# Kernel tuning notes

Measured on AMD Instinct MI355X. Metric: run time of the kernel, lower is better.

Reference implementation:

```python
import jax, jax.numpy as jnp
import numpy as np

DT = 0.025    # ms, integration time step
CM = 1.0      # uF/cm^2 membrane capacitance
E_NA, E_K, E_L = 50.0, -77.0, -54.387  # mV reversal potentials

T, N = 8192, 2048


def setup_inputs() -> dict:
    key = jax.random.key(0)
    ks = jax.random.split(key, 5)
    return {
        "input_estim": 5.0 * jax.random.normal(ks[0], (T, N), dtype=jnp.float32),  # uA/cm^2 stim per segment per step
        "V0": -65.0 + 2.0 * jax.random.normal(ks[1], (N,), dtype=jnp.float32),
        "m0": 0.05 + 0.02 * jax.random.uniform(ks[2], (N,), dtype=jnp.float32),
        "h0": 0.60 + 0.05 * jax.random.uniform(ks[3], (N,), dtype=jnp.float32),
        "n0": 0.32 + 0.05 * jax.random.uniform(ks[4], (N,), dtype=jnp.float32),
        "g_na": 120.0 * jnp.ones((N,), jnp.float32),
        "g_k": 36.0 * jnp.ones((N,), jnp.float32),
        "g_l": 0.3 * jnp.ones((N,), jnp.float32),
        "g_ax": 5.0 * jnp.ones((N,), jnp.float32),  # axial coupling conductance between neighbor segments
    }


def _rates(V):
    am = 0.1 * (V + 40.0) / (1.0 - jnp.exp(-(V + 40.0) / 10.0))
    bm = 4.0 * jnp.exp(-(V + 65.0) / 18.0)
    ah = 0.07 * jnp.exp(-(V + 65.0) / 20.0)
    bh = 1.0 / (1.0 + jnp.exp(-(V + 35.0) / 10.0))
    an = 0.01 * (V + 55.0) / (1.0 - jnp.exp(-(V + 55.0) / 10.0))
    bn = 0.125 * jnp.exp(-(V + 65.0) / 80.0)
    return am, bm, ah, bh, an, bn


def reference(input_estim, V0, m0, h0, n0, g_na, g_k, g_l, g_ax):
    def step(state, i_stim):
        V, m, h, n = state
        am, bm, ah, bh, an, bn = _rates(V)
        i_ion = (g_na * m**3 * h * (V - E_NA)
                 + g_k * n**4 * (V - E_K)
                 + g_l * (V - E_L))
        # sealed-end cable: zero-flux boundaries via edge padding
        Vp = jnp.pad(V, (1, 1), mode="edge")
        i_ax = g_ax * (Vp[:-2] + Vp[2:] - 2.0 * V)
        dV = (i_ax + i_stim - i_ion) / CM
        # total transmembrane current (capacitive + ionic) = axial + stim
        mem_cur = CM * dV + i_ion
        new_state = (V + DT * dV,
                     m + DT * (am * (1.0 - m) - bm * m),
                     h + DT * (ah * (1.0 - h) - bh * h),
                     n + DT * (an * (1.0 - n) - bn * n))
        return new_state, (mem_cur, V)

    state0 = (V0, m0, h0, n0)
    (Vf, mf, hf, nf), (mem_currents, mem_voltages) = jax.lax.scan(step, state0, input_estim)
    # (mem_currents_over_time, mem_voltage_over_time, final state)
    return mem_currents, mem_voltages, Vf, mf, hf, nf
```

## Files before the change

kernel.cpp:

```cpp
#include <hip/hip_runtime.h>

typedef unsigned long long u64;
typedef unsigned int u32;

#define TSTEPS 8192
#define NSEG   2048
#define DTC    0.025f

#define KST    28
#define KTAIL  16
#define WAVE   64
#define COWN   8
#define NBLK   (NSEG / COWN)
#define NPH    ((TSTEPS + KST - 1) / KST)
#define JLO    KST
#define LDP    66

constexpr double L2E = 1.4426950408889634074;

#define AM_A ((float)(-0.1 * L2E))
#define CEM  0.018315638888734179f
#define CEH  0.030197383422318501f
#define CEN  0.0040867714384640666f
#define BM_A ((float)(-L2E / 18.0))
#define BM_B ((float)(2.0 - 65.0 * L2E / 18.0))
#define QA   ((float)(-L2E / 80.0))
#define QB   ((float)(-65.0 * L2E / 80.0))
#define CAH  0.2645751311064591f

#define AL(p) __hip_atomic_load((p), __ATOMIC_RELAXED, __HIP_MEMORY_SCOPE_AGENT)
#define AS(p, v) __hip_atomic_store((p), (v), __ATOMIC_RELAXED, __HIP_MEMORY_SCOPE_AGENT)

__device__ __forceinline__ u64 pack_tag(float v, int tag) {
    return ((u64)(u32)tag << 32) | (u64)__float_as_uint(v);
}
__device__ __forceinline__ float lo_f(u64 w) { return __uint_as_float((u32)w); }
__device__ __forceinline__ float bperm(int addr, float v) {
    return __int_as_float(__builtin_amdgcn_ds_bpermute(addr, __float_as_int(v)));
}

template <int KS>
__device__ __forceinline__ void run_phase(
    int p, int b, int j, int s, int sc,
    bool owned, int addrL, int addrR,
    float gna, float gk, float gl, float gax,
    const float* __restrict__ stim, u64* __restrict__ tstate,
    float* __restrict__ out_cur, float* __restrict__ out_volt,
    float* lds, float& V, float& m, float& h, float& n, bool pub)
{
    const int t0 = p * KST;
    const float* sp = stim + (size_t)t0 * NSEG + sc;

    float st[KS];
#pragma unroll
    for (int k = 0; k < KS; ++k)
        st[k] = sp[(size_t)k * NSEG];
    __builtin_amdgcn_sched_barrier(0);

    const bool needLoad = (!owned) || (p == 0);
    const u64* sb = tstate + (size_t)(p & 1) * 4 * NSEG + sc;
    {
        u64 w0 = 0, w1 = 0, w2 = 0, w3 = 0;
        int ok;
        do {
            ok = 1;
            if (needLoad) {
                w0 = AL(sb);            w1 = AL(sb + NSEG);
                w2 = AL(sb + 2 * NSEG); w3 = AL(sb + 3 * NSEG);
                ok = (int)(w0 >> 32) >= p && (int)(w1 >> 32) >= p &&
                     (int)(w2 >> 32) >= p && (int)(w3 >> 32) >= p;
            }
        } while (!__all(ok));
        if (needLoad) {
            V = lo_f(w0); m = lo_f(w1); h = lo_f(w2); n = lo_f(w3);
        }
    }

    float Vl = bperm(addrL, V);
    float Vr = bperm(addrR, V);

    float2* ld2 = (float2*)lds;
#pragma unroll
    for (int k = 0; k < KS; ++k) {
        const float is = st[k];
        const float ax = (Vl + Vr) - 2.0f * V;
        const float mc = __builtin_fmaf(gax, ax, is);
        const float m3 = m * m * m;
        const float n2 = n * n;
        const float i_ion = gna * m3 * h * (V - 50.0f)
                          + gk * (n2 * n2) * (V + 77.0f)
                          + gl * (V + 54.387f);
        const float dV = mc - i_ion;
        const float Vn = __builtin_fmaf(DTC, dV, V);
        const float VlN = bperm(addrL, Vn);
        const float VrN = bperm(addrR, Vn);

        ld2[k * LDP + j] = make_float2(mc, V);

        const float em0 = __builtin_amdgcn_exp2f(V * AM_A);
        const float am  = __builtin_fmaf(0.1f, V, 4.0f) *
                          __builtin_amdgcn_rcpf(__builtin_fmaf(-CEM, em0, 1.0f));
        const float an  = __builtin_fmaf(0.01f, V, 0.55f) *
                          __builtin_amdgcn_rcpf(__builtin_fmaf(-CEN, em0, 1.0f));
        const float bh  = __builtin_amdgcn_rcpf(__builtin_fmaf(CEH, em0, 1.0f));
        const float bm  = __builtin_amdgcn_exp2f(__builtin_fmaf(V, BM_A, BM_B));
        const float q   = __builtin_amdgcn_exp2f(__builtin_fmaf(V, QA, QB));
        const float tq  = CAH * (q * q);
        const float ah  = tq * tq;
        const float bn  = 0.125f * q;

        m = __builtin_fmaf(DTC, __builtin_fmaf(-(am + bm), m, am), m);
        h = __builtin_fmaf(DTC, __builtin_fmaf(-(ah + bh), h, ah), h);
        n = __builtin_fmaf(DTC, __builtin_fmaf(-(an + bn), n, an), n);
        V = Vn; Vl = VlN; Vr = VrN;
    }

    if (pub && owned) {
        u64* pb = tstate + (size_t)((p + 1) & 1) * 4 * NSEG + s;
        AS(pb,            pack_tag(V, p + 1));
        AS(pb + NSEG,     pack_tag(m, p + 1));
        AS(pb + 2 * NSEG, pack_tag(h, p + 1));
        AS(pb + 3 * NSEG, pack_tag(n, p + 1));
    }
    __builtin_amdgcn_sched_barrier(0);

    const int sbase = b * COWN;
#pragma unroll
    for (int base = 0; base < KS * COWN; base += WAVE) {
        const int idx = base + j;
        if (idx < KS * COWN) {
            const int t  = idx >> 3;
            const int sl = idx & 7;
            const float* lp = lds + (size_t)(t * LDP + JLO + sl) * 2;
            const size_t go = (size_t)(t0 + t) * NSEG + (sbase + sl);
            __builtin_nontemporal_store(lp[0], out_cur + go);
            __builtin_nontemporal_store(lp[1], out_volt + go);
        }
    }
}

__global__ __launch_bounds__(WAVE, 1) void hh_persist(
    const float* __restrict__ stim,
    const float* __restrict__ gna_p, const float* __restrict__ gk_p,
    const float* __restrict__ gl_p,  const float* __restrict__ gax_p,
    u64* __restrict__ tstate,
    float* __restrict__ out_cur, float* __restrict__ out_volt,
    float* __restrict__ tail)
{
    const int j = threadIdx.x;
    const int b = blockIdx.x;
    const int s = b * COWN - KST + j;
    const int sc = s < 0 ? 0 : (s > NSEG - 1 ? NSEG - 1 : s);
    const bool owned = (j >= JLO) && (j < JLO + COWN);

    const int jl = (s <= 0)        ? j : (j > 0  ? j - 1 : 0);
    const int jr = (s >= NSEG - 1) ? j : (j < 63 ? j + 1 : 63);
    const int addrL = jl * 4;
    const int addrR = jr * 4;

    const float gna = gna_p[sc], gk = gk_p[sc], gl = gl_p[sc], gax = gax_p[sc];

    __shared__ float lds[KST * LDP * 2];

    float V = 0.f, m = 0.f, h = 0.f, n = 0.f;

    for (int p = 0; p < NPH - 1; ++p)
        run_phase<KST>(p, b, j, s, sc, owned, addrL, addrR, gna, gk, gl, gax,
                       stim, tstate, out_cur, out_volt, lds, V, m, h, n, true);
    run_phase<KTAIL>(NPH - 1, b, j, s, sc, owned, addrL, addrR, gna, gk, gl, gax,
                     stim, tstate, out_cur, out_volt, lds, V, m, h, n, false);

    if (owned) {
        tail[s] = V; tail[NSEG + s] = m;
        tail[2 * NSEG + s] = h; tail[3 * NSEG + s] = n;
    }
}

__global__ void hh_init(const float* __restrict__ V0, const float* __restrict__ m0,
                        const float* __restrict__ h0, const float* __restrict__ n0,
                        u64* __restrict__ tstate)
{
    const int i = blockIdx.x * blockDim.x + threadIdx.x;
    if (i < NSEG) {
        tstate[i]            = pack_tag(V0[i], 0);
        tstate[NSEG + i]     = pack_tag(m0[i], 0);
        tstate[2 * NSEG + i] = pack_tag(h0[i], 0);
        tstate[3 * NSEG + i] = pack_tag(n0[i], 0);
        u64* b1 = tstate + 4 * NSEG;
        const u64 inv = (u64)(u32)0x80000000u << 32;
        b1[i] = inv; b1[NSEG + i] = inv; b1[2 * NSEG + i] = inv; b1[3 * NSEG + i] = inv;
    }
}

extern "C" void kernel_launch(void* const* d_in, const int* in_sizes, int n_in,
                              void* d_out, int out_size, void* d_ws, size_t ws_size,
                              hipStream_t stream)
{
    const float* stim = (const float*)d_in[0];
    const float* V0   = (const float*)d_in[1];
    const float* m0   = (const float*)d_in[2];
    const float* h0   = (const float*)d_in[3];
    const float* n0   = (const float*)d_in[4];
    const float* gna  = (const float*)d_in[5];
    const float* gk   = (const float*)d_in[6];
    const float* gl   = (const float*)d_in[7];
    const float* gax  = (const float*)d_in[8];

    float* out      = (float*)d_out;
    float* out_cur  = out;
    float* out_volt = out + (size_t)TSTEPS * NSEG;
    float* tail     = out + 2 * (size_t)TSTEPS * NSEG;

    u64* tstate = (u64*)d_ws;

    hipLaunchKernelGGL(hh_init, dim3(8), dim3(256), 0, stream,
                       V0, m0, h0, n0, tstate);
    hipLaunchKernelGGL(hh_persist, dim3(NBLK), dim3(WAVE), 0, stream,
                       stim, gna, gk, gl, gax, tstate,
                       out_cur, out_volt, tail);
}
```

Measured before the change: 1.178 ms.

## Prefetch next phase's stimulus before output flush and compact LDS staging buffer

The stimulus loads for the next phase are now issued at the end of the current phase, after publishing state and before the output stores, so their latency overlaps the global stores and the inter-block spin wait instead of stalling the start of each phase. The LDS staging buffer is shrunk to only the owned lanes' values, written conditionally. Register pressure rises because the prefetched stimulus array persists across phases, and the extra phase-specialised instantiation grows code size.

```diff
diff --git a/kernel.cpp b/kernel.cpp
--- a/kernel.cpp
+++ b/kernel.cpp
@@ -14,7 +14,6 @@
 #define NBLK   (NSEG / COWN)
 #define NPH    ((TSTEPS + KST - 1) / KST)
 #define JLO    KST
-#define LDP    66
 
 constexpr double L2E = 1.4426950408889634074;
 
@@ -39,23 +38,17 @@
     return __int_as_float(__builtin_amdgcn_ds_bpermute(addr, __float_as_int(v)));
 }
 
-template <int KS>
+template <int KS, int KN>
 __device__ __forceinline__ void run_phase(
     int p, int b, int j, int s, int sc,
     bool owned, int addrL, int addrR,
     float gna, float gk, float gl, float gax,
     const float* __restrict__ stim, u64* __restrict__ tstate,
     float* __restrict__ out_cur, float* __restrict__ out_volt,
-    float* lds, float& V, float& m, float& h, float& n, bool pub)
+    float2* lbuf, float (&st)[KST],
+    float& V, float& m, float& h, float& n, bool pub)
 {
     const int t0 = p * KST;
-    const float* sp = stim + (size_t)t0 * NSEG + sc;
-
-    float st[KS];
-#pragma unroll
-    for (int k = 0; k < KS; ++k)
-        st[k] = sp[(size_t)k * NSEG];
-    __builtin_amdgcn_sched_barrier(0);
 
     const bool needLoad = (!owned) || (p == 0);
     const u64* sb = tstate + (size_t)(p & 1) * 4 * NSEG + sc;
@@ -79,7 +72,7 @@
     float Vl = bperm(addrL, V);
     float Vr = bperm(addrR, V);
 
-    float2* ld2 = (float2*)lds;
+    const int jo = j - JLO;
 #pragma unroll
     for (int k = 0; k < KS; ++k) {
         const float is = st[k];
@@ -95,7 +88,7 @@
         const float VlN = bperm(addrL, Vn);
         const float VrN = bperm(addrR, Vn);
 
-        ld2[k * LDP + j] = make_float2(mc, V);
+        if (owned) lbuf[k * COWN + jo] = make_float2(mc, V);
 
         const float em0 = __builtin_amdgcn_exp2f(V * AM_A);
         const float am  = __builtin_fmaf(0.1f, V, 4.0f) *
@@ -124,17 +117,23 @@
     }
     __builtin_amdgcn_sched_barrier(0);
 
+    if (KN > 0) {
+        const float* spn = stim + (size_t)(t0 + KST) * NSEG + sc;
+#pragma unroll
+        for (int u = 0; u < KN; ++u)
+            st[u] = spn[(size_t)u * NSEG];
+    }
+    __builtin_amdgcn_sched_barrier(0);
+
     const int sbase = b * COWN;
 #pragma unroll
     for (int base = 0; base < KS * COWN; base += WAVE) {
         const int idx = base + j;
         if (idx < KS * COWN) {
-            const int t  = idx >> 3;
-            const int sl = idx & 7;
-            const float* lp = lds + (size_t)(t * LDP + JLO + sl) * 2;
-            const size_t go = (size_t)(t0 + t) * NSEG + (sbase + sl);
-            __builtin_nontemporal_store(lp[0], out_cur + go);
-            __builtin_nontemporal_store(lp[1], out_volt + go);
+            const float2 v = lbuf[idx];
+            const size_t go = (size_t)(t0 + (idx >> 3)) * NSEG + sbase + (idx & 7);
+            __builtin_nontemporal_store(v.x, out_cur + go);
+            __builtin_nontemporal_store(v.y, out_volt + go);
         }
     }
 }
@@ -160,15 +159,26 @@
 
     const float gna = gna_p[sc], gk = gk_p[sc], gl = gl_p[sc], gax = gax_p[sc];
 
-    __shared__ float lds[KST * LDP * 2];
+    __shared__ float2 lbuf[KST * COWN];
 
     float V = 0.f, m = 0.f, h = 0.f, n = 0.f;
-
-    for (int p = 0; p < NPH - 1; ++p)
-        run_phase<KST>(p, b, j, s, sc, owned, addrL, addrR, gna, gk, gl, gax,
-                       stim, tstate, out_cur, out_volt, lds, V, m, h, n, true);
-    run_phase<KTAIL>(NPH - 1, b, j, s, sc, owned, addrL, addrR, gna, gk, gl, gax,
-                     stim, tstate, out_cur, out_volt, lds, V, m, h, n, false);
+    float st[KST];
+
+#pragma unroll
+    for (int u = 0; u < KST; ++u)
+        st[u] = stim[(size_t)u * NSEG + sc];
+    __builtin_amdgcn_sched_barrier(0);
+
+    for (int p = 0; p < NPH - 2; ++p)
+        run_phase<KST, KST>(p, b, j, s, sc, owned, addrL, addrR,
+                            gna, gk, gl, gax, stim, tstate,
+                            out_cur, out_volt, lbuf, st, V, m, h, n, true);
+    run_phase<KST, KTAIL>(NPH - 2, b, j, s, sc, owned, addrL, addrR,
+                          gna, gk, gl, gax, stim, tstate,
+                          out_cur, out_volt, lbuf, st, V, m, h, n, true);
+    run_phase<KTAIL, 0>(NPH - 1, b, j, s, sc, owned, addrL, addrR,
+                        gna, gk, gl, gax, stim, tstate,
+                        out_cur, out_volt, lbuf, st, V, m, h, n, false);
 
     if (owned) {
         tail[s] = V; tail[NSEG + s] = m;
```

Result: no change. 1.194 ms (+1.4%).

## Widen blocks to four waves with LDS neighbor exchange and staged stimulus

Applied to the files above, without the earlier changes.

Replaces 256 single-wave blocks (8 owned segments, 28-step halos) with 16 blocks of 256 threads that each own 128 segments, using 64-step phases and 64-cell halos on each side. Neighbor voltages are exchanged through shared memory with a __syncthreads every time step instead of wave-local ds_bpermute. Stimulus is staged into LDS with vectorized float4 loads, and outputs are buffered in LDS, then written back coalesced. This reduces redundant halo compute and the number of cross-block sync phases, but adds a block-wide barrier per step and uses only 16 of the device's CUs.

```diff
diff --git a/kernel.cpp b/kernel.cpp
--- a/kernel.cpp
+++ b/kernel.cpp
@@ -7,14 +7,11 @@
 #define NSEG   2048
 #define DTC    0.025f
 
-#define KST    28
-#define KTAIL  16
-#define WAVE   64
-#define COWN   8
+#define NT     256
+#define KST    64
+#define COWN   128
 #define NBLK   (NSEG / COWN)
-#define NPH    ((TSTEPS + KST - 1) / KST)
-#define JLO    KST
-#define LDP    66
+#define NPH    (TSTEPS / KST)
 
 constexpr double L2E = 1.4426950408889634074;
 
@@ -35,111 +32,11 @@
     return ((u64)(u32)tag << 32) | (u64)__float_as_uint(v);
 }
 __device__ __forceinline__ float lo_f(u64 w) { return __uint_as_float((u32)w); }
-__device__ __forceinline__ float bperm(int addr, float v) {
-    return __int_as_float(__builtin_amdgcn_ds_bpermute(addr, __float_as_int(v)));
-}
-
-template <int KS>
-__device__ __forceinline__ void run_phase(
-    int p, int b, int j, int s, int sc,
-    bool owned, int addrL, int addrR,
-    float gna, float gk, float gl, float gax,
-    const float* __restrict__ stim, u64* __restrict__ tstate,
-    float* __restrict__ out_cur, float* __restrict__ out_volt,
-    float* lds, float& V, float& m, float& h, float& n, bool pub)
-{
-    const int t0 = p * KST;
-    const float* sp = stim + (size_t)t0 * NSEG + sc;
-
-    float st[KS];
-#pragma unroll
-    for (int k = 0; k < KS; ++k)
-        st[k] = sp[(size_t)k * NSEG];
-    __builtin_amdgcn_sched_barrier(0);
-
-    const bool needLoad = (!owned) || (p == 0);
-    const u64* sb = tstate + (size_t)(p & 1) * 4 * NSEG + sc;
-    {
-        u64 w0 = 0, w1 = 0, w2 = 0, w3 = 0;
-        int ok;
-        do {
-            ok = 1;
-            if (needLoad) {
-                w0 = AL(sb);            w1 = AL(sb + NSEG);
-                w2 = AL(sb + 2 * NSEG); w3 = AL(sb + 3 * NSEG);
-                ok = (int)(w0 >> 32) >= p && (int)(w1 >> 32) >= p &&
-                     (int)(w2 >> 32) >= p && (int)(w3 >> 32) >= p;
-            }
-        } while (!__all(ok));
-        if (needLoad) {
-            V = lo_f(w0); m = lo_f(w1); h = lo_f(w2); n = lo_f(w3);
-        }
-    }
-
-    float Vl = bperm(addrL, V);
-    float Vr = bperm(addrR, V);
-
-    float2* ld2 = (float2*)lds;
-#pragma unroll
-    for (int k = 0; k < KS; ++k) {
-        const float is = st[k];
-        const float ax = (Vl + Vr) - 2.0f * V;
-        const float mc = __builtin_fmaf(gax, ax, is);
-        const float m3 = m * m * m;
-        const float n2 = n * n;
-        const float i_ion = gna * m3 * h * (V - 50.0f)
-                          + gk * (n2 * n2) * (V + 77.0f)
-                          + gl * (V + 54.387f);
-        const float dV = mc - i_ion;
-        const float Vn = __builtin_fmaf(DTC, dV, V);
-        const float VlN = bperm(addrL, Vn);
-        const float VrN = bperm(addrR, Vn);
-
-        ld2[k * LDP + j] = make_float2(mc, V);
-
-        const float em0 = __builtin_amdgcn_exp2f(V * AM_A);
-        const float am  = __builtin_fmaf(0.1f, V, 4.0f) *
-                          __builtin_amdgcn_rcpf(__builtin_fmaf(-CEM, em0, 1.0f));
-        const float an  = __builtin_fmaf(0.01f, V, 0.55f) *
-                          __builtin_amdgcn_rcpf(__builtin_fmaf(-CEN, em0, 1.0f));
-        const float bh  = __builtin_amdgcn_rcpf(__builtin_fmaf(CEH, em0, 1.0f));
-        const float bm  = __builtin_amdgcn_exp2f(__builtin_fmaf(V, BM_A, BM_B));
-        const float q   = __builtin_amdgcn_exp2f(__builtin_fmaf(V, QA, QB));
-        const float tq  = CAH * (q * q);
-        const float ah  = tq * tq;
-        const float bn  = 0.125f * q;
-
-        m = __builtin_fmaf(DTC, __builtin_fmaf(-(am + bm), m, am), m);
-        h = __builtin_fmaf(DTC, __builtin_fmaf(-(ah + bh), h, ah), h);
-        n = __builtin_fmaf(DTC, __builtin_fmaf(-(an + bn), n, an), n);
-        V = Vn; Vl = VlN; Vr = VrN;
-    }
-
-    if (pub && owned) {
-        u64* pb = tstate + (size_t)((p + 1) & 1) * 4 * NSEG + s;
-        AS(pb,            pack_tag(V, p + 1));
-        AS(pb + NSEG,     pack_tag(m, p + 1));
-        AS(pb + 2 * NSEG, pack_tag(h, p + 1));
-        AS(pb + 3 * NSEG, pack_tag(n, p + 1));
-    }
-    __builtin_amdgcn_sched_barrier(0);
-
-    const int sbase = b * COWN;
-#pragma unroll
-    for (int base = 0; base < KS * COWN; base += WAVE) {
-        const int idx = base + j;
-        if (idx < KS * COWN) {
-            const int t  = idx >> 3;
-            const int sl = idx & 7;
-            const float* lp = lds + (size_t)(t * LDP + JLO + sl) * 2;
-            const size_t go = (size_t)(t0 + t) * NSEG + (sbase + sl);
-            __builtin_nontemporal_store(lp[0], out_cur + go);
-            __builtin_nontemporal_store(lp[1], out_volt + go);
-        }
-    }
-}
-
-__global__ __launch_bounds__(WAVE, 1) void hh_persist(
+__device__ __forceinline__ int clampi(int x) {
+    return x < 0 ? 0 : (x > NSEG - 1 ? NSEG - 1 : x);
+}
+
+__global__ __launch_bounds__(NT, 1) void hh_persist(
     const float* __restrict__ stim,
     const float* __restrict__ gna_p, const float* __restrict__ gk_p,
     const float* __restrict__ gl_p,  const float* __restrict__ gax_p,
@@ -147,30 +44,131 @@
     float* __restrict__ out_cur, float* __restrict__ out_volt,
     float* __restrict__ tail)
 {
-    const int j = threadIdx.x;
-    const int b = blockIdx.x;
-    const int s = b * COWN - KST + j;
-    const int sc = s < 0 ? 0 : (s > NSEG - 1 ? NSEG - 1 : s);
-    const bool owned = (j >= JLO) && (j < JLO + COWN);
-
-    const int jl = (s <= 0)        ? j : (j > 0  ? j - 1 : 0);
-    const int jr = (s >= NSEG - 1) ? j : (j < 63 ? j + 1 : 63);
-    const int addrL = jl * 4;
-    const int addrR = jr * 4;
+    const int tid = threadIdx.x;
+    const int b   = blockIdx.x;
+    const int s   = b * COWN - KST + tid;
+    const int sc  = clampi(s);
+    const int wid = tid >> 6;
+    const bool ownedWave = (wid == 1) || (wid == 2);
+    const int jl = (s <= 0)        ? tid : (tid > 0      ? tid - 1 : tid);
+    const int jr = (s >= NSEG - 1) ? tid : (tid < NT - 1 ? tid + 1 : tid);
 
     const float gna = gna_p[sc], gk = gk_p[sc], gl = gl_p[sc], gax = gax_p[sc];
 
-    __shared__ float lds[KST * LDP * 2];
+    __shared__ float  stimS[KST * NT];
+    __shared__ float2 outS[KST * COWN];
+    __shared__ float  vx[2][NT];
 
     float V = 0.f, m = 0.f, h = 0.f, n = 0.f;
 
-    for (int p = 0; p < NPH - 1; ++p)
-        run_phase<KST>(p, b, j, s, sc, owned, addrL, addrR, gna, gk, gl, gax,
-                       stim, tstate, out_cur, out_volt, lds, V, m, h, n, true);
-    run_phase<KTAIL>(NPH - 1, b, j, s, sc, owned, addrL, addrR, gna, gk, gl, gax,
-                     stim, tstate, out_cur, out_volt, lds, V, m, h, n, false);
-
-    if (owned) {
+    for (int p = 0; p < NPH; ++p) {
+        const int t0 = p * KST;
+
+        {
+            const size_t tb = (size_t)t0 * NSEG;
+            const int col = (tid & 63) << 2;
+            const int sg  = b * COWN - KST + col;
+            float4 stg[16];
+            if (sg >= 0 && sg <= NSEG - 4) {
+#pragma unroll
+                for (int i = 0; i < 16; ++i)
+                    stg[i] = *(const float4*)(stim + tb + (size_t)(4*i + wid) * NSEG + sg);
+            } else {
+#pragma unroll
+                for (int i = 0; i < 16; ++i) {
+                    const float* r = stim + tb + (size_t)(4*i + wid) * NSEG;
+                    stg[i].x = r[clampi(sg)];     stg[i].y = r[clampi(sg + 1)];
+                    stg[i].z = r[clampi(sg + 2)]; stg[i].w = r[clampi(sg + 3)];
+                }
+            }
+            __builtin_amdgcn_sched_barrier(0);
+#pragma unroll
+            for (int i = 0; i < 16; ++i)
+                *(float4*)&stimS[(4*i + wid) * NT + col] = stg[i];
+        }
+
+        const bool needLoad = (!ownedWave) || (p == 0);
+        const u64* sb = tstate + (size_t)(p & 1) * 4 * NSEG + sc;
+        {
+            u64 w0 = 0, w1 = 0, w2 = 0, w3 = 0;
+            int ok;
+            do {
+                ok = 1;
+                if (needLoad) {
+                    w0 = AL(sb);            w1 = AL(sb + NSEG);
+                    w2 = AL(sb + 2 * NSEG); w3 = AL(sb + 3 * NSEG);
+                    ok = (int)(w0 >> 32) >= p && (int)(w1 >> 32) >= p &&
+                         (int)(w2 >> 32) >= p && (int)(w3 >> 32) >= p;
+                }
+            } while (!__all(ok));
+            if (needLoad) {
+                V = lo_f(w0); m = lo_f(w1); h = lo_f(w2); n = lo_f(w3);
+            }
+        }
+
+        vx[0][tid] = V;
+        __syncthreads();
+        float Vl = vx[0][jl];
+        float Vr = vx[0][jr];
+
+#pragma unroll 4
+        for (int k = 0; k < KST; ++k) {
+            const float is = stimS[k * NT + tid];
+            const float ax = (Vl + Vr) - 2.0f * V;
+            const float mc = __builtin_fmaf(gax, ax, is);
+            const float m3 = m * m * m;
+            const float n2 = n * n;
+            const float i_ion = gna * m3 * h * (V - 50.0f)
+                              + gk * (n2 * n2) * (V + 77.0f)
+                              + gl * (V + 54.387f);
+            const float dV = mc - i_ion;
+            const float Vn = __builtin_fmaf(DTC, dV, V);
+
+            vx[(k + 1) & 1][tid] = Vn;
+            __syncthreads();
+            const float VlN = vx[(k + 1) & 1][jl];
+            const float VrN = vx[(k + 1) & 1][jr];
+            if (ownedWave) outS[k * COWN + (tid - 64)] = make_float2(mc, V);
+
+            const float em0 = __builtin_amdgcn_exp2f(V * AM_A);
+            const float am  = __builtin_fmaf(0.1f, V, 4.0f) *
+                              __builtin_amdgcn_rcpf(__builtin_fmaf(-CEM, em0, 1.0f));
+            const float an  = __builtin_fmaf(0.01f, V, 0.55f) *
+                              __builtin_amdgcn_rcpf(__builtin_fmaf(-CEN, em0, 1.0f));
+            const float bh  = __builtin_amdgcn_rcpf(__builtin_fmaf(CEH, em0, 1.0f));
+            const float bm  = __builtin_amdgcn_exp2f(__builtin_fmaf(V, BM_A, BM_B));
+            const float q   = __builtin_amdgcn_exp2f(__builtin_fmaf(V, QA, QB));
+            const float tq  = CAH * (q * q);
+            const float ah  = tq * tq;
+            const float bn  = 0.125f * q;
+
+            m = __builtin_fmaf(DTC, __builtin_fmaf(-(am + bm), m, am), m);
+            h = __builtin_fmaf(DTC, __builtin_fmaf(-(ah + bh), h, ah), h);
+            n = __builtin_fmaf(DTC, __builtin_fmaf(-(an + bn), n, an), n);
+            V = Vn; Vl = VlN; Vr = VrN;
+        }
+
+        if ((p + 1 < NPH) && ownedWave) {
+            u64* pb = tstate + (size_t)((p + 1) & 1) * 4 * NSEG + s;
+            AS(pb,            pack_tag(V, p + 1));
+            AS(pb + NSEG,     pack_tag(m, p + 1));
+            AS(pb + 2 * NSEG, pack_tag(h, p + 1));
+            AS(pb + 3 * NSEG, pack_tag(n, p + 1));
+        }
+        __builtin_amdgcn_sched_barrier(0);
+
+#pragma unroll
+        for (int i = 0; i < (KST * COWN) / NT; ++i) {
+            const int e  = i * NT + tid;
+            const float2 v = outS[e];
+            const size_t go = (size_t)(t0 + (e >> 7)) * NSEG + b * COWN + (e & 127);
+            __builtin_nontemporal_store(v.x, out_cur + go);
+            __builtin_nontemporal_store(v.y, out_volt + go);
+        }
+        __syncthreads();
+    }
+
+    if (ownedWave) {
         tail[s] = V; tail[NSEG + s] = m;
         tail[2 * NSEG + s] = h; tail[3 * NSEG + s] = n;
     }
@@ -215,7 +213,7 @@
 
     hipLaunchKernelGGL(hh_init, dim3(8), dim3(256), 0, stream,
                        V0, m0, h0, n0, tstate);
-    hipLaunchKernelGGL(hh_persist, dim3(NBLK), dim3(WAVE), 0, stream,
+    hipLaunchKernelGGL(hh_persist, dim3(NBLK), dim3(NT), 0, stream,
                        stim, gna, gk, gl, gax, tstate,
                        out_cur, out_volt, tail);
 }
```

Result: slower. 2.301 ms (+95.3%).
